# Performance work log

Measured on AMD Instinct MI355X. Metric: run time of the kernel, lower is better.

Reference implementation:

```python
import jax, jax.numpy as jnp
import numpy as np

N_QUBITS = 8
N_LAYERS = 3
B = 8192
IN_DIM = 84 * 84  # 7056
FEAT = 2 ** N_QUBITS  # 256
HID = 128
N_ACTIONS = 6


def _apply_1q(st, gate, w):
    # st: (B, 2**n) complex; gate: (2,2) or (B,2,2); wire w (wire 0 = MSB)
    Bn = st.shape[0]
    st = st.reshape(Bn, 2 ** w, 2, -1)
    sub = 'ab,sxby->sxay' if gate.ndim == 2 else 'sab,sxby->sxay'
    return jnp.einsum(sub, gate, st).reshape(Bn, -1)


def _apply_cnot(st, c, t):
    # control c < target t
    Bn = st.shape[0]
    st = st.reshape(Bn, 2 ** c, 2, 2 ** (t - c - 1), 2, -1)
    c0 = st[:, :, 0]                      # (B, 2**c, mid, 2, rest)
    c1 = jnp.flip(st[:, :, 1], axis=3)    # flip target bit where control=1
    return jnp.stack([c0, c1], axis=2).reshape(Bn, -1)


def _ry(theta):
    c = jnp.cos(theta / 2)
    s = jnp.sin(theta / 2)
    g = jnp.stack([jnp.stack([c, -s], -1), jnp.stack([s, c], -1)], -2)
    return g.astype(jnp.complex64)


def _rx(theta):
    c = jnp.cos(theta / 2).astype(jnp.complex64)
    s = (-1j) * jnp.sin(theta / 2).astype(jnp.complex64)
    return jnp.stack([jnp.stack([c, s], -1), jnp.stack([s, c], -1)], -2)


def _rz(theta):
    tc = theta.astype(jnp.complex64)
    em = jnp.exp(-0.5j * tc)
    ep = jnp.exp(0.5j * tc)
    z = jnp.zeros_like(em)
    return jnp.stack([jnp.stack([em, z], -1), jnp.stack([z, ep], -1)], -2)


def _simulate(angles, qparams):
    # angles: (B, N_QUBITS) float; qparams: (N_LAYERS, N_QUBITS, 3)
    n = N_QUBITS
    Bn = angles.shape[0]
    H = jnp.asarray(np.array([[1, 1], [1, -1]], np.complex64) / np.sqrt(2))
    state = jnp.zeros((Bn, 2 ** n), jnp.complex64).at[:, 0].set(1.0)
    # encoding: H then RY(inputs[i]*pi) on each wire (per-sample angles)
    for i in range(n):
        state = _apply_1q(state, H, i)
        state = _apply_1q(state, _ry(angles[:, i] * np.float32(np.pi)), i)
    # variational layers
    for layer in range(N_LAYERS):
        for i in range(0, n - 1, 2):
            state = _apply_cnot(state, i, i + 1)
        for i in range(1, n - 1, 2):
            state = _apply_cnot(state, i, i + 1)
        for i in range(n):
            state = _apply_1q(state, _rx(qparams[layer, i, 0]), i)
            state = _apply_1q(state, _ry(qparams[layer, i, 1]), i)
            state = _apply_1q(state, _rz(qparams[layer, i, 2]), i)
    probs = state.real ** 2 + state.imag ** 2  # (B, 2**n)
    sign = jnp.array([1.0, -1.0], jnp.float32)
    evs = [
        (probs.reshape(Bn, 2 ** i, 2, -1) * sign[None, None, :, None]).sum((1, 2, 3))
        for i in range(n)
    ]
    return jnp.stack(evs, axis=1)  # (B, n) <Z_i>


def setup_inputs() -> dict:
    key = jax.random.key(0)
    ks = jax.random.split(key, 8)
    rn = lambda k, shape, s: jax.random.normal(k, shape, jnp.float32) * s
    return {
        'x': rn(ks[0], (B, IN_DIM), 1.0),
        'pre_W1': rn(ks[1], (IN_DIM, 512), 0.01),
        'pre_b1': jnp.zeros((512,), jnp.float32),
        'pre_W2': rn(ks[2], (512, FEAT), 0.04),
        'pre_b2': jnp.zeros((FEAT,), jnp.float32),
        'qparams': rn(ks[3], (N_LAYERS, N_QUBITS, 3), 0.1),
        'post_W1': rn(ks[4], (N_QUBITS, HID), 0.2),
        'post_b1': jnp.zeros((HID,), jnp.float32),
        'post_W2': rn(ks[5], (HID, HID // 2), 0.08),
        'post_b2': jnp.zeros((HID // 2,), jnp.float32),
        'post_W3': rn(ks[6], (HID // 2, N_ACTIONS), 0.1),
        'post_b3': jnp.zeros((N_ACTIONS,), jnp.float32),
    }


def reference(x, pre_W1, pre_b1, pre_W2, pre_b2, qparams,
              post_W1, post_b1, post_W2, post_b2, post_W3, post_b3):
    # classical preprocess (dropout = identity in eval)
    h = jax.nn.relu(x @ pre_W1 + pre_b1)
    feats = jnp.tanh(h @ pre_W2 + pre_b2)        # (B, 256)
    # quantum circuit only consumes the first N_QUBITS feature entries
    q = _simulate(feats[:, :N_QUBITS], qparams)  # (B, 8)
    h2 = jax.nn.relu(q @ post_W1 + post_b1)
    h3 = jax.nn.relu(h2 @ post_W2 + post_b2)
    return h3 @ post_W3 + post_b3                # (B, 6) Q-values
```

## Files before the change

kernel.cpp:

```cpp
#include <hip/hip_runtime.h>

typedef _Float16 half_t;
typedef _Float16 v8h __attribute__((ext_vector_type(8)));
typedef __fp16 pk2 __attribute__((ext_vector_type(2)));
typedef float v4f __attribute__((ext_vector_type(4)));

#define KIN 7056
#define KP 7072
#define GM 8192
#define GN 512
#define SLICE (8192L * 512)

__device__ __forceinline__ void async16(const void* g, void* l) {
  __builtin_amdgcn_global_load_lds((const __attribute__((address_space(1))) void*)g,
                                   (__attribute__((address_space(3))) void*)l, 16, 0, 0);
}

__global__ __launch_bounds__(256) void conv_w1t(const float* __restrict__ W1, half_t* __restrict__ w1t) {
  __shared__ float t[32][65];
  int tid = threadIdx.x;
  int k0 = blockIdx.x * 32;
  int n0 = blockIdx.y * 64;
  #pragma unroll
  for (int rr = 0; rr < 8; rr++) {
    int r = rr * 4 + (tid >> 6);
    int c = tid & 63;
    int k = k0 + r;
    t[r][c] = (k < KIN) ? W1[(long)k * GN + n0 + c] : 0.f;
  }
  __syncthreads();
  int n_l = tid >> 2;
  int k_l = (tid & 3) * 8;
  v8h o;
  #pragma unroll
  for (int j = 0; j < 8; j++) o[j] = (_Float16)t[k_l + j][n_l];
  *(v8h*)&w1t[(long)(n0 + n_l) * KP + k0 + k_l] = o;
}

__global__ __launch_bounds__(256) void small_setup(const float* __restrict__ W2, const float* __restrict__ qp,
                                                   float* __restrict__ w2c, float* __restrict__ umat) {
  int t = threadIdx.x;
  for (int i = t; i < 512; i += 256) {
    #pragma unroll
    for (int j = 0; j < 8; j++) w2c[i * 8 + j] = W2[i * 256 + j];
  }
  if (t < 24) {
    float a2 = qp[t * 3 + 0] * 0.5f;
    float b2 = qp[t * 3 + 1] * 0.5f;
    float g2 = qp[t * 3 + 2] * 0.5f;
    float ca = cosf(a2), sa = sinf(a2);
    float cb = cosf(b2), sb = sinf(b2);
    float cg = cosf(g2), sg = sinf(g2);
    float m00r = cb * ca, m00i =  sb * sa;
    float m01r = -sb * ca, m01i = -cb * sa;
    float m10r =  sb * ca, m10i = -cb * sa;
    float m11r =  cb * ca, m11i = -sb * sa;
    float* u = umat + t * 8;
    u[0] = m00r * cg + m00i * sg;  u[1] = m00i * cg - m00r * sg;
    u[2] = m01r * cg + m01i * sg;  u[3] = m01i * cg - m01r * sg;
    u[4] = m10r * cg - m10i * sg;  u[5] = m10i * cg + m10r * sg;
    u[6] = m11r * cg - m11i * sg;  u[7] = m11i * cg + m11r * sg;
  }
}

__global__ __launch_bounds__(256, 3) void gemm1(const float* __restrict__ A, const half_t* __restrict__ B,
                                                float* __restrict__ P) {
  __shared__ float  Ash[128 * 32];
  __shared__ half_t Bsh[128 * 32];
  int tid = threadIdx.x, lane = tid & 63, wave = tid >> 6;
  int bid = blockIdx.x;
  int n0 = (bid / 192) * 128;
  int p  = bid % 192;
  int kc = p % 3;
  int m0 = (p / 3) * 128;
  int kbeg = kc * 2368;
  int kend = (kc == 2) ? KP : kbeg + 2368;
  int wm = (wave & 1) * 64;
  int wn = (wave >> 1) * 64;
  int lrow = lane & 15;
  int lkg = lane >> 4;

  int c4 = tid & 7;
  int rA0 = tid >> 3;
  int c8 = tid & 3;
  int rB0 = tid >> 2;
  long Arow[4]; int Asc[4];
  #pragma unroll
  for (int rr = 0; rr < 4; rr++) {
    int r = rr * 32 + rA0;
    Arow[rr] = (long)(m0 + r) * KIN;
    Asc[rr] = (c4 ^ (r & 7)) * 4;
  }
  const half_t* Bg[2];
  #pragma unroll
  for (int rr = 0; rr < 2; rr++) {
    int r = rr * 64 + rB0;
    Bg[rr] = B + (long)(n0 + r) * KP + (c8 ^ (r & 3)) * 8;
  }
  float* AsD[4]; half_t* BsD[2];
  #pragma unroll
  for (int rr = 0; rr < 4; rr++) AsD[rr] = &Ash[(rr * 256 + tid) * 4];
  #pragma unroll
  for (int rr = 0; rr < 2; rr++) BsD[rr] = &Bsh[(rr * 256 + tid) * 8];

  v4f acc[4][4];
  #pragma unroll
  for (int i = 0; i < 4; i++)
    #pragma unroll
    for (int j = 0; j < 4; j++)
      acc[i][j] = (v4f){0.f, 0.f, 0.f, 0.f};

  for (int k0 = kbeg; k0 < kend; k0 += 32) {
    #pragma unroll
    for (int rr = 0; rr < 4; rr++) {
      int col = k0 + Asc[rr];
      col = col > 7052 ? 7052 : col;
      async16(A + Arow[rr] + col, AsD[rr]);
    }
    #pragma unroll
    for (int rr = 0; rr < 2; rr++) async16(Bg[rr] + k0, BsD[rr]);
    asm volatile("s_waitcnt vmcnt(0)" ::: "memory");
    __syncthreads();

    v8h af[4], bf[4];
    #pragma unroll
    for (int i = 0; i < 4; i++) {
      int row = wm + i * 16 + lrow;
      int sw = row & 7;
      int c4a = lkg * 2;
      v4f lo = *(const v4f*)&Ash[row * 32 + ((c4a ^ sw) * 4)];
      v4f hi = *(const v4f*)&Ash[row * 32 + (((c4a + 1) ^ sw) * 4)];
      union { v8h v; pk2 h[4]; } u;
      u.h[0] = __builtin_amdgcn_cvt_pkrtz(lo[0], lo[1]);
      u.h[1] = __builtin_amdgcn_cvt_pkrtz(lo[2], lo[3]);
      u.h[2] = __builtin_amdgcn_cvt_pkrtz(hi[0], hi[1]);
      u.h[3] = __builtin_amdgcn_cvt_pkrtz(hi[2], hi[3]);
      af[i] = u.v;
    }
    #pragma unroll
    for (int j = 0; j < 4; j++) {
      int row = wn + j * 16 + lrow;
      bf[j] = *(const v8h*)&Bsh[row * 32 + ((lkg ^ (row & 3)) * 8)];
    }
    #pragma unroll
    for (int i = 0; i < 4; i++)
      #pragma unroll
      for (int j = 0; j < 4; j++)
        acc[i][j] = __builtin_amdgcn_mfma_f32_16x16x32_f16(af[i], bf[j], acc[i][j], 0, 0, 0);
    __syncthreads();
  }

  float* Pk = P + kc * SLICE;
  int crow = lkg * 4;
  #pragma unroll
  for (int j = 0; j < 4; j++) {
    int col = n0 + wn + j * 16 + lrow;
    #pragma unroll
    for (int i = 0; i < 4; i++) {
      int rbase = m0 + wm + i * 16 + crow;
      #pragma unroll
      for (int v = 0; v < 4; v++)
        Pk[(long)(rbase + v) * GN + col] = acc[i][j][v];
    }
  }
}

__device__ __forceinline__ void cnot_lane(float ar[4], float ai[4], int lane, int cm, int tm) {
  bool c = (lane & cm) != 0;
  #pragma unroll
  for (int r = 0; r < 4; r++) {
    float pr = __shfl_xor(ar[r], tm);
    float pi = __shfl_xor(ai[r], tm);
    ar[r] = c ? pr : ar[r];
    ai[r] = c ? pi : ai[r];
  }
}

__device__ __forceinline__ void rot_lane(float ar[4], float ai[4], int lane, int mk, const float u[8]) {
  bool hi = (lane & mk) != 0;
  float csr = hi ? u[6] : u[0], csi = hi ? u[7] : u[1];
  float cpr = hi ? u[4] : u[2], cpi = hi ? u[5] : u[3];
  #pragma unroll
  for (int r = 0; r < 4; r++) {
    float pr = __shfl_xor(ar[r], mk);
    float pi = __shfl_xor(ai[r], mk);
    float nr = csr * ar[r] - csi * ai[r] + cpr * pr - cpi * pi;
    float ni = csr * ai[r] + csi * ar[r] + cpr * pi + cpi * pr;
    ar[r] = nr; ai[r] = ni;
  }
}

__device__ __forceinline__ void apply2(const float u[8], float& x0r, float& x0i, float& x1r, float& x1i) {
  float n0r = u[0] * x0r - u[1] * x0i + u[2] * x1r - u[3] * x1i;
  float n0i = u[0] * x0i + u[1] * x0r + u[2] * x1i + u[3] * x1r;
  float n1r = u[4] * x0r - u[5] * x0i + u[6] * x1r - u[7] * x1i;
  float n1i = u[4] * x0i + u[5] * x0r + u[6] * x1i + u[7] * x1r;
  x0r = n0r; x0i = n0i; x1r = n1r; x1i = n1i;
}

__global__ __launch_bounds__(256) void quantum_post(
    const float* __restrict__ P, const float* __restrict__ b1, const float* __restrict__ w2c,
    const float* __restrict__ b2, const float* __restrict__ umat,
    const float* __restrict__ W1p, const float* __restrict__ b1p,
    const float* __restrict__ W2p, const float* __restrict__ b2p,
    const float* __restrict__ W3p, const float* __restrict__ b3p,
    float* __restrict__ out) {
  __shared__ float h2s[4][128];
  int tid = threadIdx.x;
  int wave = tid >> 6, lane = tid & 63;
  int s = blockIdx.x * 4 + wave;

  long base = (long)s * GN + lane * 8;
  v4f h0 = (v4f){0.f,0.f,0.f,0.f}, h1 = h0;
  #pragma unroll
  for (int c = 0; c < 3; c++) {
    h0 += *(const v4f*)&P[c * SLICE + base];
    h1 += *(const v4f*)&P[c * SLICE + base + 4];
  }
  float hk[8];
  #pragma unroll
  for (int t = 0; t < 4; t++) hk[t]     = fmaxf(h0[t] + b1[lane * 8 + t], 0.f);
  #pragma unroll
  for (int t = 0; t < 4; t++) hk[t + 4] = fmaxf(h1[t] + b1[lane * 8 + 4 + t], 0.f);
  float a[8] = {0,0,0,0,0,0,0,0};
  const float* w2r = w2c + lane * 64;
  #pragma unroll
  for (int t = 0; t < 8; t++) {
    v4f wlo = *(const v4f*)&w2r[t * 8];
    v4f whi = *(const v4f*)&w2r[t * 8 + 4];
    #pragma unroll
    for (int j = 0; j < 4; j++) { a[j] += hk[t] * wlo[j]; a[j + 4] += hk[t] * whi[j]; }
  }
  #pragma unroll
  for (int m = 1; m < 64; m <<= 1)
    #pragma unroll
    for (int j = 0; j < 8; j++) a[j] += __shfl_xor(a[j], m);
  float f[8];
  #pragma unroll
  for (int j = 0; j < 8; j++) f[j] = tanhf(a[j] + b2[j]);

  float v0[8], v1[8];
  #pragma unroll
  for (int q = 0; q < 8; q++) {
    float ang = f[q] * 1.57079632679f;
    float sn, cs;
    __sincosf(ang, &sn, &cs);
    v0[q] = (cs - sn) * 0.70710678118f;
    v1[q] = (cs + sn) * 0.70710678118f;
  }
  float ar[4], ai[4];
  #pragma unroll
  for (int r = 0; r < 4; r++) {
    int i = lane * 4 + r;
    float prod = 1.f;
    #pragma unroll
    for (int q = 0; q < 8; q++) prod *= ((i >> (7 - q)) & 1) ? v1[q] : v0[q];
    ar[r] = prod; ai[r] = 0.f;
  }

  #pragma unroll
  for (int L = 0; L < 3; L++) {
    cnot_lane(ar, ai, lane, 32, 16);
    cnot_lane(ar, ai, lane, 8, 4);
    cnot_lane(ar, ai, lane, 2, 1);
    { float t = ar[2]; ar[2] = ar[3]; ar[3] = t; t = ai[2]; ai[2] = ai[3]; ai[3] = t; }
    cnot_lane(ar, ai, lane, 16, 8);
    cnot_lane(ar, ai, lane, 4, 2);
    {
      bool c = (lane & 1) != 0;
      #pragma unroll
      for (int r = 0; r < 2; r++) {
        float t0 = ar[r], t1 = ar[r + 2];
        ar[r] = c ? t1 : t0; ar[r + 2] = c ? t0 : t1;
        t0 = ai[r]; t1 = ai[r + 2];
        ai[r] = c ? t1 : t0; ai[r + 2] = c ? t0 : t1;
      }
    }
    #pragma unroll
    for (int q = 0; q < 6; q++) {
      float u[8];
      #pragma unroll
      for (int c = 0; c < 8; c++) u[c] = umat[(L * 8 + q) * 8 + c];
      rot_lane(ar, ai, lane, 32 >> q, u);
    }
    {
      float u[8];
      #pragma unroll
      for (int c = 0; c < 8; c++) u[c] = umat[(L * 8 + 6) * 8 + c];
      apply2(u, ar[0], ai[0], ar[2], ai[2]);
      apply2(u, ar[1], ai[1], ar[3], ai[3]);
      #pragma unroll
      for (int c = 0; c < 8; c++) u[c] = umat[(L * 8 + 7) * 8 + c];
      apply2(u, ar[0], ai[0], ar[1], ai[1]);
      apply2(u, ar[2], ai[2], ar[3], ai[3]);
    }
  }

  float p0 = ar[0] * ar[0] + ai[0] * ai[0];
  float p1 = ar[1] * ar[1] + ai[1] * ai[1];
  float p2 = ar[2] * ar[2] + ai[2] * ai[2];
  float p3 = ar[3] * ar[3] + ai[3] * ai[3];
  float psum = p0 + p1 + p2 + p3;
  float e[8];
  #pragma unroll
  for (int q = 0; q < 6; q++) e[q] = (lane & (32 >> q)) ? -psum : psum;
  e[6] = p0 + p1 - p2 - p3;
  e[7] = p0 - p1 + p2 - p3;
  #pragma unroll
  for (int m = 1; m < 64; m <<= 1)
    #pragma unroll
    for (int q = 0; q < 8; q++) e[q] += __shfl_xor(e[q], m);

  float h2a = b1p[lane], h2b = b1p[lane + 64];
  #pragma unroll
  for (int k = 0; k < 8; k++) {
    h2a += e[k] * W1p[k * 128 + lane];
    h2b += e[k] * W1p[k * 128 + lane + 64];
  }
  h2s[wave][lane] = fmaxf(h2a, 0.f);
  h2s[wave][lane + 64] = fmaxf(h2b, 0.f);
  __syncthreads();
  float h3 = b2p[lane];
  #pragma unroll 8
  for (int k = 0; k < 128; k++) h3 += h2s[wave][k] * W2p[k * 64 + lane];
  h3 = fmaxf(h3, 0.f);
  float o[6];
  #pragma unroll
  for (int j = 0; j < 6; j++) o[j] = h3 * W3p[lane * 6 + j];
  #pragma unroll
  for (int m = 1; m < 64; m <<= 1)
    #pragma unroll
    for (int j = 0; j < 6; j++) o[j] += __shfl_xor(o[j], m);
  if (lane == 0) {
    #pragma unroll
    for (int j = 0; j < 6; j++) out[(long)s * 6 + j] = o[j] + b3p[j];
  }
}

extern "C" void kernel_launch(void* const* d_in, const int* in_sizes, int n_in,
                              void* d_out, int out_size, void* d_ws, size_t ws_size,
                              hipStream_t stream) {
  const float* x   = (const float*)d_in[0];
  const float* W1  = (const float*)d_in[1];
  const float* b1  = (const float*)d_in[2];
  const float* W2  = (const float*)d_in[3];
  const float* b2  = (const float*)d_in[4];
  const float* qp  = (const float*)d_in[5];
  const float* W1p = (const float*)d_in[6];
  const float* b1p = (const float*)d_in[7];
  const float* W2p = (const float*)d_in[8];
  const float* b2p = (const float*)d_in[9];
  const float* W3p = (const float*)d_in[10];
  const float* b3p = (const float*)d_in[11];
  float* out = (float*)d_out;

  char* ws = (char*)d_ws;
  half_t* w1t  = (half_t*)(ws);
  float*  w2c  = (float*)(ws + 7241728);
  float*  umat = (float*)(ws + 7258112);
  float*  P    = (float*)(ws + 7258880);

  conv_w1t<<<dim3(221, 8), 256, 0, stream>>>(W1, w1t);
  small_setup<<<1, 256, 0, stream>>>(W2, qp, w2c, umat);
  gemm1<<<768, 256, 0, stream>>>(x, w1t, P);
  quantum_post<<<2048, 256, 0, stream>>>(P, b1, w2c, b2, umat,
                                         W1p, b1p, W2p, b2p, W3p, b3p, out);
}
```

Measured before the change: 467.3 us.

## Double-buffer GEMM1 with register-staged fp16 A conversion and 4-way split-K

The main GEMM changes from a single-buffered loop that async-loads fp32 A into LDS to a double-buffered pipeline. The next A tile is loaded into registers, converted to fp16, and stored to the other LDS buffer while the current tile feeds the MFMAs; B is prefetched asynchronously the same way. This halves A's LDS footprint and overlaps global loads with compute. K is repadded to 7168 and split into 4 equal segments across 1024 blocks with a new block-to-tile mapping, and the post kernel now sums 4 partial slices with a coalesced access pattern and a fast exp-based tanh. The costs are an extra partial-sum slice to write and read, and the fast tanh loses a little accuracy.

```diff
diff --git a/kernel.cpp b/kernel.cpp
--- a/kernel.cpp
+++ b/kernel.cpp
@@ -6,9 +6,11 @@
 typedef float v4f __attribute__((ext_vector_type(4)));
 
 #define KIN 7056
-#define KP 7072
+#define KP2 7168
 #define GM 8192
 #define GN 512
+#define KSEG 1792
+#define NSTEP 56
 #define SLICE (8192L * 512)
 
 __device__ __forceinline__ void async16(const void* g, void* l) {
@@ -34,7 +36,7 @@
   v8h o;
   #pragma unroll
   for (int j = 0; j < 8; j++) o[j] = (_Float16)t[k_l + j][n_l];
-  *(v8h*)&w1t[(long)(n0 + n_l) * KP + k0 + k_l] = o;
+  *(v8h*)&w1t[(long)(n0 + n_l) * KP2 + k0 + k_l] = o;
 }
 
 __global__ __launch_bounds__(256) void small_setup(const float* __restrict__ W2, const float* __restrict__ qp,
@@ -63,45 +65,34 @@
   }
 }
 
-__global__ __launch_bounds__(256, 3) void gemm1(const float* __restrict__ A, const half_t* __restrict__ B,
+__global__ __launch_bounds__(256, 4) void gemm1(const float* __restrict__ A, const half_t* __restrict__ B,
                                                 float* __restrict__ P) {
-  __shared__ float  Ash[128 * 32];
-  __shared__ half_t Bsh[128 * 32];
+  __shared__ half_t Ash[2][128 * 32];
+  __shared__ half_t Bsh[2][128 * 32];
   int tid = threadIdx.x, lane = tid & 63, wave = tid >> 6;
   int bid = blockIdx.x;
-  int n0 = (bid / 192) * 128;
-  int p  = bid % 192;
-  int kc = p % 3;
-  int m0 = (p / 3) * 128;
-  int kbeg = kc * 2368;
-  int kend = (kc == 2) ? KP : kbeg + 2368;
+  int m0 = (bid & 63) * 128;
+  int g = bid >> 6;
+  int n0 = (g & 3) * 128;
+  int kc = g >> 2;
+  int kbeg = kc * KSEG;
+
   int wm = (wave & 1) * 64;
   int wn = (wave >> 1) * 64;
   int lrow = lane & 15;
   int lkg = lane >> 4;
 
-  int c4 = tid & 7;
-  int rA0 = tid >> 3;
-  int c8 = tid & 3;
-  int rB0 = tid >> 2;
-  long Arow[4]; int Asc[4];
-  #pragma unroll
-  for (int rr = 0; rr < 4; rr++) {
-    int r = rr * 32 + rA0;
-    Arow[rr] = (long)(m0 + r) * KIN;
-    Asc[rr] = (c4 ^ (r & 7)) * 4;
-  }
-  const half_t* Bg[2];
+  long abase[2]; int acol[2];
+  const half_t* bsrc[2];
   #pragma unroll
   for (int rr = 0; rr < 2; rr++) {
-    int r = rr * 64 + rB0;
-    Bg[rr] = B + (long)(n0 + r) * KP + (c8 ^ (r & 3)) * 8;
-  }
-  float* AsD[4]; half_t* BsD[2];
-  #pragma unroll
-  for (int rr = 0; rr < 4; rr++) AsD[rr] = &Ash[(rr * 256 + tid) * 4];
-  #pragma unroll
-  for (int rr = 0; rr < 2; rr++) BsD[rr] = &Bsh[(rr * 256 + tid) * 8];
+    int s = rr * 256 + tid;
+    int row = s >> 2;
+    int csrc = (s & 3) ^ ((row >> 1) & 3);
+    abase[rr] = (long)(m0 + row) * KIN;
+    acol[rr] = csrc * 8;
+    bsrc[rr] = B + (long)(n0 + row) * KP2 + kbeg + csrc * 8;
+  }
 
   v4f acc[4][4];
   #pragma unroll
@@ -110,43 +101,70 @@
     for (int j = 0; j < 4; j++)
       acc[i][j] = (v4f){0.f, 0.f, 0.f, 0.f};
 
-  for (int k0 = kbeg; k0 < kend; k0 += 32) {
-    #pragma unroll
-    for (int rr = 0; rr < 4; rr++) {
-      int col = k0 + Asc[rr];
-      col = col > 7052 ? 7052 : col;
-      async16(A + Arow[rr] + col, AsD[rr]);
-    }
-    #pragma unroll
-    for (int rr = 0; rr < 2; rr++) async16(Bg[rr] + k0, BsD[rr]);
-    asm volatile("s_waitcnt vmcnt(0)" ::: "memory");
-    __syncthreads();
+  v4f ra[2][2];
+  #pragma unroll
+  for (int rr = 0; rr < 2; rr++) {
+    int col = kbeg + acol[rr];
+    col = col > KIN - 8 ? KIN - 8 : col;
+    const float* src = A + abase[rr] + col;
+    ra[rr][0] = *(const v4f*)src;
+    ra[rr][1] = *(const v4f*)(src + 4);
+  }
+  #pragma unroll
+  for (int rr = 0; rr < 2; rr++) async16(bsrc[rr], &Bsh[0][(rr * 256 + tid) * 8]);
+  #pragma unroll
+  for (int rr = 0; rr < 2; rr++) {
+    union { v8h v; pk2 h[4]; } u;
+    u.h[0] = __builtin_amdgcn_cvt_pkrtz(ra[rr][0][0], ra[rr][0][1]);
+    u.h[1] = __builtin_amdgcn_cvt_pkrtz(ra[rr][0][2], ra[rr][0][3]);
+    u.h[2] = __builtin_amdgcn_cvt_pkrtz(ra[rr][1][0], ra[rr][1][1]);
+    u.h[3] = __builtin_amdgcn_cvt_pkrtz(ra[rr][1][2], ra[rr][1][3]);
+    *(v8h*)&Ash[0][(rr * 256 + tid) * 8] = u.v;
+  }
+  asm volatile("s_waitcnt vmcnt(0)" ::: "memory");
+  __syncthreads();
+
+  for (int k = 0; k < NSTEP; k++) {
+    int p = k & 1;
+    int kn = (k + 1 < NSTEP) ? (k + 1) : k;
+    int kofs = kbeg + kn * 32;
+    #pragma unroll
+    for (int rr = 0; rr < 2; rr++) {
+      int col = kofs + acol[rr];
+      col = col > KIN - 8 ? KIN - 8 : col;
+      const float* src = A + abase[rr] + col;
+      ra[rr][0] = *(const v4f*)src;
+      ra[rr][1] = *(const v4f*)(src + 4);
+    }
+    #pragma unroll
+    for (int rr = 0; rr < 2; rr++) async16(bsrc[rr] + kn * 32, &Bsh[1 - p][(rr * 256 + tid) * 8]);
 
     v8h af[4], bf[4];
     #pragma unroll
     for (int i = 0; i < 4; i++) {
       int row = wm + i * 16 + lrow;
-      int sw = row & 7;
-      int c4a = lkg * 2;
-      v4f lo = *(const v4f*)&Ash[row * 32 + ((c4a ^ sw) * 4)];
-      v4f hi = *(const v4f*)&Ash[row * 32 + (((c4a + 1) ^ sw) * 4)];
-      union { v8h v; pk2 h[4]; } u;
-      u.h[0] = __builtin_amdgcn_cvt_pkrtz(lo[0], lo[1]);
-      u.h[1] = __builtin_amdgcn_cvt_pkrtz(lo[2], lo[3]);
-      u.h[2] = __builtin_amdgcn_cvt_pkrtz(hi[0], hi[1]);
-      u.h[3] = __builtin_amdgcn_cvt_pkrtz(hi[2], hi[3]);
-      af[i] = u.v;
+      af[i] = *(const v8h*)&Ash[p][row * 32 + (lkg ^ ((row >> 1) & 3)) * 8];
     }
     #pragma unroll
     for (int j = 0; j < 4; j++) {
       int row = wn + j * 16 + lrow;
-      bf[j] = *(const v8h*)&Bsh[row * 32 + ((lkg ^ (row & 3)) * 8)];
+      bf[j] = *(const v8h*)&Bsh[p][row * 32 + (lkg ^ ((row >> 1) & 3)) * 8];
     }
     #pragma unroll
     for (int i = 0; i < 4; i++)
       #pragma unroll
       for (int j = 0; j < 4; j++)
         acc[i][j] = __builtin_amdgcn_mfma_f32_16x16x32_f16(af[i], bf[j], acc[i][j], 0, 0, 0);
+
+    #pragma unroll
+    for (int rr = 0; rr < 2; rr++) {
+      union { v8h v; pk2 h[4]; } u;
+      u.h[0] = __builtin_amdgcn_cvt_pkrtz(ra[rr][0][0], ra[rr][0][1]);
+      u.h[1] = __builtin_amdgcn_cvt_pkrtz(ra[rr][0][2], ra[rr][0][3]);
+      u.h[2] = __builtin_amdgcn_cvt_pkrtz(ra[rr][1][0], ra[rr][1][1]);
+      u.h[3] = __builtin_amdgcn_cvt_pkrtz(ra[rr][1][2], ra[rr][1][3]);
+      *(v8h*)&Ash[1 - p][(rr * 256 + tid) * 8] = u.v;
+    }
     __syncthreads();
   }
 
@@ -210,26 +228,19 @@
   int wave = tid >> 6, lane = tid & 63;
   int s = blockIdx.x * 4 + wave;
 
-  long base = (long)s * GN + lane * 8;
-  v4f h0 = (v4f){0.f,0.f,0.f,0.f}, h1 = h0;
-  #pragma unroll
-  for (int c = 0; c < 3; c++) {
-    h0 += *(const v4f*)&P[c * SLICE + base];
-    h1 += *(const v4f*)&P[c * SLICE + base + 4];
-  }
-  float hk[8];
-  #pragma unroll
-  for (int t = 0; t < 4; t++) hk[t]     = fmaxf(h0[t] + b1[lane * 8 + t], 0.f);
-  #pragma unroll
-  for (int t = 0; t < 4; t++) hk[t + 4] = fmaxf(h1[t] + b1[lane * 8 + 4 + t], 0.f);
-  float a[8] = {0,0,0,0,0,0,0,0};
-  const float* w2r = w2c + lane * 64;
-  #pragma unroll
-  for (int t = 0; t < 8; t++) {
-    v4f wlo = *(const v4f*)&w2r[t * 8];
-    v4f whi = *(const v4f*)&w2r[t * 8 + 4];
-    #pragma unroll
-    for (int j = 0; j < 4; j++) { a[j] += hk[t] * wlo[j]; a[j + 4] += hk[t] * whi[j]; }
+  long pbase = (long)s * GN + lane;
+  float a[8] = {0, 0, 0, 0, 0, 0, 0, 0};
+  #pragma unroll
+  for (int m = 0; m < 8; m++) {
+    int i = lane + 64 * m;
+    float hv = b1[i];
+    #pragma unroll
+    for (int c = 0; c < 4; c++) hv += P[c * SLICE + pbase + 64 * m];
+    hv = fmaxf(hv, 0.f);
+    v4f wlo = *(const v4f*)&w2c[i * 8];
+    v4f whi = *(const v4f*)&w2c[i * 8 + 4];
+    #pragma unroll
+    for (int j = 0; j < 4; j++) { a[j] += hv * wlo[j]; a[j + 4] += hv * whi[j]; }
   }
   #pragma unroll
   for (int m = 1; m < 64; m <<= 1)
@@ -237,7 +248,11 @@
     for (int j = 0; j < 8; j++) a[j] += __shfl_xor(a[j], m);
   float f[8];
   #pragma unroll
-  for (int j = 0; j < 8; j++) f[j] = tanhf(a[j] + b2[j]);
+  for (int j = 0; j < 8; j++) {
+    float z = a[j] + b2[j];
+    float ex = __expf(2.f * z);
+    f[j] = 1.f - 2.f / (ex + 1.f);
+  }
 
   float v0[8], v1[8];
   #pragma unroll
@@ -356,13 +371,13 @@
 
   char* ws = (char*)d_ws;
   half_t* w1t  = (half_t*)(ws);
-  float*  w2c  = (float*)(ws + 7241728);
-  float*  umat = (float*)(ws + 7258112);
-  float*  P    = (float*)(ws + 7258880);
-
-  conv_w1t<<<dim3(221, 8), 256, 0, stream>>>(W1, w1t);
+  float*  w2c  = (float*)(ws + 7340032);
+  float*  umat = (float*)(ws + 7356416);
+  float*  P    = (float*)(ws + 7357440);
+
+  conv_w1t<<<dim3(224, 8), 256, 0, stream>>>(W1, w1t);
   small_setup<<<1, 256, 0, stream>>>(W2, qp, w2c, umat);
-  gemm1<<<768, 256, 0, stream>>>(x, w1t, P);
+  gemm1<<<1024, 256, 0, stream>>>(x, w1t, P);
   quantum_post<<<2048, 256, 0, stream>>>(P, b1, w2c, b2, umat,
                                          W1p, b1p, W2p, b2p, W3p, b3p, out);
 }
```

Result: slower. 484.2 us (+3.6%).
